# Kernel tuning notes

Measured on AMD Instinct MI355X. Metric: run time of the kernel, lower is better.

## Reference

```python
import jax, jax.numpy as jnp
import numpy as np

N_NODES = 50000
N_EDGES = 800000
F_IN, F_MID, F_OUT = 256, 128, 40


def gcn_conv(x, W, b, src, dst, n_nodes):
    # GCNConv (PyG defaults): add self-loops, symmetric normalization,
    # linear transform, scatter-sum to targets, then bias.
    h = x @ W  # [N, F_out]
    loop = jnp.arange(n_nodes, dtype=src.dtype)
    s = jnp.concatenate([src, loop])  # sources incl. self-loops
    d = jnp.concatenate([dst, loop])  # targets incl. self-loops
    deg = jax.ops.segment_sum(jnp.ones_like(d, dtype=h.dtype), d, num_segments=n_nodes)
    dinv = jnp.where(deg > 0, jax.lax.rsqrt(deg), 0.0)
    norm = dinv[s] * dinv[d]  # [E+N]
    msgs = h[s] * norm[:, None]  # [E+N, F_out]
    out = jax.ops.segment_sum(msgs, d, num_segments=n_nodes)
    return out + b


def setup_inputs() -> dict:
    key = jax.random.key(0)
    ks = jax.random.split(key, 8)
    x = jax.random.normal(ks[0], (N_NODES, F_IN), dtype=jnp.float32)
    edge_index = jax.random.randint(ks[1], (2, N_EDGES), 0, N_NODES, dtype=jnp.int64)

    def glorot(k, fin, fout):
        lim = float(np.sqrt(6.0 / (fin + fout)))
        return jax.random.uniform(k, (fin, fout), jnp.float32, -lim, lim)

    return {
        "x": x,
        "edge_index": edge_index,
        "W_in": glorot(ks[2], F_IN, F_MID),
        "b_in": jnp.zeros((F_MID,), jnp.float32),
        "W_mid": glorot(ks[3], F_MID, F_MID),
        "b_mid": jnp.zeros((F_MID,), jnp.float32),
        "W_out": glorot(ks[4], F_MID, F_OUT),
        "b_out": jnp.zeros((F_OUT,), jnp.float32),
    }


def reference(x, edge_index, W_in, b_in, W_mid, b_mid, W_out, b_out):
    src, dst = edge_index[0], edge_index[1]
    n = x.shape[0]
    # conv_in -> relu (dropout is identity in eval mode)
    h = jax.nn.relu(gcn_conv(x, W_in, b_in, src, dst, n))
    # middle GCN layer -> relu
    h = jax.nn.relu(gcn_conv(h, W_mid, b_mid, src, dst, n))
    # conv_out -> log_softmax over classes
    h = gcn_conv(h, W_out, b_out, src, dst, n)
    return jax.nn.log_softmax(h, axis=-1)
```

## Files before the change

### kernel.cpp

```cpp
#include <hip/hip_runtime.h>
#include <hip/hip_bf16.h>
#include <math.h>


#define F_IN  256
#define F_MID 128
#define F_OUT 40
#define PSH   9
#define BCAP2 10240

typedef __attribute__((ext_vector_type(8))) short bf16x8;
typedef __attribute__((ext_vector_type(4))) float f32x4;

union FragU {
    bf16x8 v;
    __hip_bfloat162 h2[4];
    uint4 u;
    unsigned short s[8];
};

__device__ __forceinline__ unsigned int f2bf(float f) {
    unsigned int u = __float_as_uint(f);
    return (u + 0x7fffu + ((u >> 16) & 1u)) >> 16;
}
__device__ __forceinline__ float bf_lo(unsigned int u) { return __uint_as_float(u << 16); }
__device__ __forceinline__ float bf_hi(unsigned int u) { return __uint_as_float(u & 0xffff0000u); }

__device__ __forceinline__ void add_row(float* acc, uint4 u) {
    acc[0] += bf_lo(u.x); acc[1] += bf_hi(u.x);
    acc[2] += bf_lo(u.y); acc[3] += bf_hi(u.y);
    acc[4] += bf_lo(u.z); acc[5] += bf_hi(u.z);
    acc[6] += bf_lo(u.w); acc[7] += bf_hi(u.w);
}

__global__ __launch_bounds__(256) void k_bucket_prep(const int* __restrict__ src,
                                                     const int* __restrict__ dst,
                                                     unsigned int* __restrict__ bkt,
                                                     int* __restrict__ bcur,
                                                     int E, int nbBkt,
                                                     const float* __restrict__ W1,
                                                     const float* __restrict__ W2,
                                                     const float* __restrict__ W3,
                                                     unsigned short* __restrict__ Wp1,
                                                     unsigned short* __restrict__ Wp2,
                                                     unsigned short* __restrict__ Wp3) {
    if (blockIdx.x >= (unsigned)nbBkt) {
        int t = (blockIdx.x - nbBkt) * 256 + threadIdx.x;
        const float* W; unsigned short* Wp; int M, Mp, kc, nn;
        if (t < 4096)      { W = W1; Wp = Wp1; M = 128; Mp = 128; kc = t >> 7; nn = t & 127; }
        else if (t < 6144) { t -= 4096; W = W2; Wp = Wp2; M = 128; Mp = 128; kc = t >> 7; nn = t & 127; }
        else if (t < 6912) { t -= 6144; W = W3; Wp = Wp3; M = 40;  Mp = 48;  kc = t / 48; nn = t % 48; }
        else return;
        FragU o;
#pragma unroll
        for (int j = 0; j < 8; ++j) {
            int k = kc * 8 + j;
            o.s[j] = (nn < M) ? (unsigned short)f2bf(W[k * M + nn]) : 0;
        }
        *(uint4*)&Wp[((size_t)kc * Mp + nn) * 8] = o.u;
        return;
    }
    __shared__ int hist[128], base[128], cur[128];
    const int t = threadIdx.x;
    if (t < 128) { hist[t] = 0; cur[t] = 0; }
    __syncthreads();
    const int e0 = blockIdx.x * 8192;
    unsigned int mye[32];
#pragma unroll
    for (int j = 0; j < 32; ++j) {
        int e = e0 + j * 256 + t;
        if (e < E) {
            mye[j] = ((unsigned int)dst[e] << 16) | (unsigned int)src[e];
            atomicAdd(&hist[mye[j] >> (16 + PSH)], 1);
        } else mye[j] = 0xffffffffu;
    }
    __syncthreads();
    if (t < 128) base[t] = hist[t] ? atomicAdd(&bcur[t], hist[t]) : 0;
    __syncthreads();
#pragma unroll
    for (int j = 0; j < 32; ++j) {
        if (mye[j] != 0xffffffffu) {
            int p = mye[j] >> (16 + PSH);
            int pos = base[p] + atomicAdd(&cur[p], 1);
            if (pos < BCAP2) bkt[(size_t)p * BCAP2 + pos] = mye[j];
        }
    }
}

__global__ __launch_bounds__(256) void k_sort_pref(const unsigned int* __restrict__ bkt,
                                                   const int* __restrict__ bcur,
                                                   int* __restrict__ rofs,
                                                   float* __restrict__ dinv,
                                                   unsigned short* __restrict__ csr,
                                                   int npart, int n,
                                                   const float* __restrict__ x,
                                                   int nbPref,
                                                   unsigned short* __restrict__ hn1,
                                                   unsigned short* __restrict__ hn2,
                                                   unsigned short* __restrict__ hn3) {
    __shared__ int sh[768];
    if (blockIdx.x >= (unsigned)npart) {
        const int b = blockIdx.x - npart;
        const float4* xp = (const float4*)x;
        const int total4 = n * 64;
        for (int i = b * 256 + threadIdx.x; i < total4; i += nbPref * 256) {
            float4 v = xp[i];
            asm volatile("" :: "v"(v.x), "v"(v.y), "v"(v.z), "v"(v.w));
        }
        return;
    }
    int* hist = sh;
    int* stmp = sh + 512;
    const int p = blockIdx.x;
    const int t = threadIdx.x;
    const int d0 = p << PSH;
    const int nd = min(512, n - d0);

    if (p == 0) {
        uint4 z = make_uint4(0, 0, 0, 0);
        if (t < 16) *(uint4*)(hn1 + (size_t)n * 128 + t * 8) = z;
        else if (t < 32) *(uint4*)(hn2 + (size_t)n * 128 + (t - 16) * 8) = z;
        else if (t < 52) ((unsigned int*)(hn3 + (size_t)n * 40))[t - 32] = 0;
    }

    int bv = (t < p) ? bcur[t] : 0;
    bv = bv > BCAP2 ? BCAP2 : bv;
    stmp[t] = bv;
    hist[t] = 0; hist[t + 256] = 0;
    __syncthreads();
#pragma unroll
    for (int off = 128; off; off >>= 1) {
        if (t < off) stmp[t] += stmp[t + off];
        __syncthreads();
    }
    const int base = stmp[0];
    int np = bcur[p]; np = np > BCAP2 ? BCAP2 : np;
    const unsigned int* b = bkt + (size_t)p * BCAP2;

    for (int i0 = t; i0 < np; i0 += 2048) {
        unsigned int ee[8];
#pragma unroll
        for (int j = 0; j < 8; ++j) {
            int idx = i0 + j * 256;
            ee[j] = (idx < np) ? b[idx] : 0xffffffffu;
        }
#pragma unroll
        for (int j = 0; j < 8; ++j)
            if (ee[j] != 0xffffffffu)
                atomicAdd(&hist[(int)(ee[j] >> 16) - d0], 1);
    }
    __syncthreads();

    const int h0 = hist[2 * t], h1 = hist[2 * t + 1];
    __syncthreads();
    stmp[t] = h0 + h1;
    __syncthreads();
#pragma unroll
    for (int off = 1; off < 256; off <<= 1) {
        int xx = (t >= off) ? stmp[t - off] : 0;
        __syncthreads();
        stmp[t] += xx;
        __syncthreads();
    }
    const int excl = stmp[t] - (h0 + h1);

    hist[2 * t] = excl;
    hist[2 * t + 1] = excl + h0;
    if (2 * t < nd) {
        rofs[d0 + 2 * t] = base + excl;
        dinv[d0 + 2 * t] = rsqrtf((float)(h0 + 1));
    }
    if (2 * t + 1 < nd) {
        rofs[d0 + 2 * t + 1] = base + excl + h0;
        dinv[d0 + 2 * t + 1] = rsqrtf((float)(h1 + 1));
    }
    if (p == npart - 1 && t == 0) rofs[n] = base + np;
    __syncthreads();

    for (int i0 = t; i0 < np; i0 += 2048) {
        unsigned int ee[8];
#pragma unroll
        for (int j = 0; j < 8; ++j) {
            int idx = i0 + j * 256;
            ee[j] = (idx < np) ? b[idx] : 0xffffffffu;
        }
#pragma unroll
        for (int j = 0; j < 8; ++j) {
            if (ee[j] != 0xffffffffu) {
                int ld = (int)(ee[j] >> 16) - d0;
                int pos = atomicAdd(&hist[ld], 1);
                csr[base + pos] = (unsigned short)(ee[j] & 0xffffu);
            }
        }
    }
}

__global__ __launch_bounds__(256) void k_gemm1s(const float* __restrict__ x,
                                                const unsigned short* __restrict__ Wp1,
                                                const float* __restrict__ dinv,
                                                unsigned short* __restrict__ hn, int n) {
    const int t = threadIdx.x;
    const int w = t >> 6, lane = t & 63, sub = lane & 15, q = lane >> 4;
    const int row0 = blockIdx.x * 64 + w * 16;
    const int row = row0 + sub;
    const bool rv = row < n;
    const float* ap = x + (size_t)row * 256;

    float4 xv[16];
    if (rv) {
#pragma unroll
        for (int j = 0; j < 16; ++j)
            xv[j] = *(const float4*)(ap + (j >> 1) * 32 + q * 8 + (j & 1) * 4);
    } else {
#pragma unroll
        for (int j = 0; j < 16; ++j) xv[j] = make_float4(0.f, 0.f, 0.f, 0.f);
    }

    f32x4 acc[8];
#pragma unroll
    for (int cg = 0; cg < 8; ++cg) acc[cg] = (f32x4)0.f;

#pragma unroll
    for (int kk = 0; kk < 8; ++kk) {
        FragU af;
        float4 f0 = xv[2 * kk];
        float4 f1 = xv[2 * kk + 1];
        af.h2[0] = __float22bfloat162_rn(make_float2(f0.x, f0.y));
        af.h2[1] = __float22bfloat162_rn(make_float2(f0.z, f0.w));
        af.h2[2] = __float22bfloat162_rn(make_float2(f1.x, f1.y));
        af.h2[3] = __float22bfloat162_rn(make_float2(f1.z, f1.w));
        const unsigned short* wrow = Wp1 + (size_t)((kk * 4 + q) * 128 + sub) * 8;
#pragma unroll
        for (int cg = 0; cg < 8; ++cg) {
            bf16x8 b = *(const bf16x8*)(wrow + cg * 16 * 8);
            acc[cg] = __builtin_amdgcn_mfma_f32_16x16x32_bf16(b, af.v, acc[cg], 0, 0, 0);
        }
    }
    if (rv) {
        float dv = dinv[row];
#pragma unroll
        for (int cg = 0; cg < 8; ++cg) {
            uint2 pk;
            pk.x = f2bf(dv * acc[cg][0]) | (f2bf(dv * acc[cg][1]) << 16);
            pk.y = f2bf(dv * acc[cg][2]) | (f2bf(dv * acc[cg][3]) << 16);
            *(uint2*)(hn + (size_t)row * 128 + cg * 16 + q * 4) = pk;
        }
    }
}

template <int MOUT, int MP>
__global__ __launch_bounds__(256) void k_agg_gemm(const unsigned short* __restrict__ hnS,
                                                  const int* __restrict__ rofs,
                                                  const unsigned short* __restrict__ csr,
                                                  const float* __restrict__ dinv,
                                                  const float* __restrict__ bias,
                                                  const unsigned short* __restrict__ Wp,
                                                  unsigned short* __restrict__ hout,
                                                  int n) {
    __shared__ unsigned short arows[16][136];
    const int t = threadIdx.x;
    const int w = t >> 6, lane = t & 63, sub = lane & 15, q = lane >> 4;
    const int v0 = blockIdx.x * 16;
    const int r = w * 4 + q;
    const int node = v0 + r;
    const bool nv = node < n;

    float acc[8];
#pragma unroll
    for (int k = 0; k < 8; ++k) acc[k] = 0.f;

    int e0 = 0, deg = 0;
    if (nv) { e0 = rofs[node]; deg = rofs[node + 1] - e0; }
    const int total = nv ? deg + 1 : 0;
    int ea = (sub < deg) ? (int)csr[e0 + sub] : n;
    int eb = (16 + sub < deg) ? (int)csr[e0 + 16 + sub] : n;
    const int lim = (total < 33) ? total : 33;

    for (int ix0 = 0; ix0 < lim; ix0 += 8) {
        int sA[8];
#pragma unroll
        for (int jj = 0; jj < 8; ++jj) {
            int ix = ix0 + jj;
            int em = (ix - 1) & 15;
            int srcA = __shfl(ea, (lane & 48) + em);
            int srcB = __shfl(eb, (lane & 48) + em);
            int s = (ix - 1 < 16) ? srcA : srcB;
            s = (ix == 0) ? node : s;
            sA[jj] = (ix < lim) ? s : n;
        }
        uint4 u[8];
#pragma unroll
        for (int jj = 0; jj < 8; ++jj)
            u[jj] = *(const uint4*)(hnS + (size_t)sA[jj] * 128 + sub * 8);
#pragma unroll
        for (int jj = 0; jj < 8; ++jj) add_row(acc, u[jj]);
    }
    for (int ix = 33; ix < total; ++ix) {
        int s = (int)csr[e0 + ix - 1];
        uint4 u = *(const uint4*)(hnS + (size_t)s * 128 + sub * 8);
        add_row(acc, u);
    }

    uint4 pk = make_uint4(0, 0, 0, 0);
    if (nv) {
        float dv = dinv[node];
        float4 b0 = *(const float4*)(bias + sub * 8);
        float4 b1 = *(const float4*)(bias + sub * 8 + 4);
        float o0 = fmaxf(dv * acc[0] + b0.x, 0.f);
        float o1 = fmaxf(dv * acc[1] + b0.y, 0.f);
        float o2 = fmaxf(dv * acc[2] + b0.z, 0.f);
        float o3 = fmaxf(dv * acc[3] + b0.w, 0.f);
        float o4 = fmaxf(dv * acc[4] + b1.x, 0.f);
        float o5 = fmaxf(dv * acc[5] + b1.y, 0.f);
        float o6 = fmaxf(dv * acc[6] + b1.z, 0.f);
        float o7 = fmaxf(dv * acc[7] + b1.w, 0.f);
        pk.x = f2bf(o0) | (f2bf(o1) << 16);
        pk.y = f2bf(o2) | (f2bf(o3) << 16);
        pk.z = f2bf(o4) | (f2bf(o5) << 16);
        pk.w = f2bf(o6) | (f2bf(o7) << 16);
    }
    *(uint4*)&arows[r][sub * 8] = pk;
    __syncthreads();

    const int NCG = MP / 16;
    const int NCGW = (MP == 128) ? 2 : 1;
    f32x4 gacc[2];
#pragma unroll
    for (int i = 0; i < 2; ++i) gacc[i] = (f32x4)0.f;

#pragma unroll
    for (int kstep = 0; kstep < 4; ++kstep) {
        FragU af;
        af.u = *(const uint4*)&arows[sub][kstep * 32 + q * 8];
#pragma unroll
        for (int i = 0; i < NCGW; ++i) {
            int cg = w * NCGW + i;
            if (cg < NCG) {
                bf16x8 b = *(const bf16x8*)(Wp + (size_t)((kstep * 4 + q) * MP + cg * 16 + sub) * 8);
                gacc[i] = __builtin_amdgcn_mfma_f32_16x16x32_bf16(b, af.v, gacc[i], 0, 0, 0);
            }
        }
    }
    const int orow = v0 + sub;
    if (orow < n) {
        float dvr = dinv[orow];
#pragma unroll
        for (int i = 0; i < NCGW; ++i) {
            int cg = w * NCGW + i;
            int feat = cg * 16 + q * 4;
            if (cg < NCG && feat < MOUT) {
                uint2 p2;
                p2.x = f2bf(dvr * gacc[i][0]) | (f2bf(dvr * gacc[i][1]) << 16);
                p2.y = f2bf(dvr * gacc[i][2]) | (f2bf(dvr * gacc[i][3]) << 16);
                *(uint2*)(hout + (size_t)orow * MOUT + feat) = p2;
            }
        }
    }
}

__global__ __launch_bounds__(256) void agg40_lsm_bf16(const unsigned short* __restrict__ hnS,
                                                      const int* __restrict__ rofs,
                                                      const unsigned short* __restrict__ csr,
                                                      const float* __restrict__ dinv,
                                                      const float* __restrict__ bias,
                                                      float* __restrict__ out, int n) {
    int wid = (blockIdx.x * 256 + threadIdx.x) >> 6;
    if (wid >= n) return;
    const int v = wid;
    const int lane = threadIdx.x & 63;
    const int h = lane >> 5;
    const int sl = lane & 31;
    const bool act = sl < 20;
    float a0 = 0.f, a1 = 0.f;
    const int e0 = rofs[v];
    const int total = rofs[v + 1] - e0 + 1;

    for (int i0 = 0; i0 < total; i0 += 16) {
        int sA[8];
#pragma unroll
        for (int j = 0; j < 8; ++j) {
            int ix = i0 + h + 2 * j;
            int s = (ix < total) ? ((ix == 0) ? v : (int)csr[e0 + ix - 1]) : n;
            sA[j] = s;
        }
        if (act) {
#pragma unroll
            for (int j = 0; j < 8; ++j) {
                unsigned int u = *(const unsigned int*)(hnS + (size_t)sA[j] * 40 + sl * 2);
                a0 += bf_lo(u);
                a1 += bf_hi(u);
            }
        }
    }
    a0 += __shfl_xor(a0, 32);
    a1 += __shfl_xor(a1, 32);
    float dv = dinv[v];
    float v0 = act ? (dv * a0 + bias[sl * 2])     : -3.402823466e38f;
    float v1 = act ? (dv * a1 + bias[sl * 2 + 1]) : -3.402823466e38f;
    float m = fmaxf(v0, v1);
#pragma unroll
    for (int off = 16; off; off >>= 1) m = fmaxf(m, __shfl_xor(m, off));
    float p = act ? (__expf(v0 - m) + __expf(v1 - m)) : 0.f;
#pragma unroll
    for (int off = 16; off; off >>= 1) p += __shfl_xor(p, off);
    if (h == 0 && act) {
        float ls = __logf(p);
        *(float2*)(out + (size_t)v * 40 + sl * 2) = make_float2(v0 - m - ls, v1 - m - ls);
    }
}


extern "C" void kernel_launch(void* const* d_in, const int* in_sizes, int n_in,
                              void* d_out, int out_size, void* d_ws, size_t ws_size,
                              hipStream_t stream) {
    const float* x     = (const float*)d_in[0];
    const int*   ei    = (const int*)d_in[1];
    const float* W_in  = (const float*)d_in[2];
    const float* b_in  = (const float*)d_in[3];
    const float* W_mid = (const float*)d_in[4];
    const float* b_mid = (const float*)d_in[5];
    const float* W_out = (const float*)d_in[6];
    const float* b_out = (const float*)d_in[7];
    float* out = (float*)d_out;

    const int N = in_sizes[0] / F_IN;
    const int E = in_sizes[1] / 2;
    const int* srcp = ei;
    const int* dstp = ei + E;
    const int npart = (N + (1 << PSH) - 1) >> PSH;

    char* w = (char*)d_ws;
    unsigned short* hn1 = (unsigned short*)w; w += (size_t)(N + 1) * 128 * 2;
    unsigned short* hn2 = (unsigned short*)w; w += (size_t)(N + 1) * 128 * 2;
    unsigned short* hn3 = (unsigned short*)w; w += (size_t)(N + 1) * 40 * 2 + 16;
    float* dinv = (float*)w; w += (size_t)N * 4;
    int* bcur   = (int*)w;   w += 512;
    int* rofs   = (int*)w;   w += (size_t)(N + 1) * 4 + 12;
    unsigned int* bkt = (unsigned int*)w; w += (size_t)npart * BCAP2 * 4;
    unsigned short* csr = (unsigned short*)w; w += (size_t)E * 2 + 128;
    unsigned short* Wp1 = (unsigned short*)((((size_t)w) + 15) & ~(size_t)15); w = (char*)Wp1 + 32 * 128 * 8 * 2;
    unsigned short* Wp2 = (unsigned short*)w; w += 16 * 128 * 8 * 2;
    unsigned short* Wp3 = (unsigned short*)w; w += 16 * 48 * 8 * 2;

    const int nbW = (N * 64 + 255) / 256;
    const int nbG = (N + 63) / 64;
    const int nbF = (N + 15) / 16;
    const int nbBkt = (E + 8191) / 8192;
    const int nbPref = 256;

    hipMemsetAsync(bcur, 0, 512, stream);
    k_bucket_prep<<<nbBkt + 27, 256, 0, stream>>>(srcp, dstp, bkt, bcur, E, nbBkt,
                                                  W_in, W_mid, W_out, Wp1, Wp2, Wp3);
    k_sort_pref<<<npart + nbPref, 256, 0, stream>>>(bkt, bcur, rofs, dinv, csr,
                                                    npart, N, x, nbPref, hn1, hn2, hn3);
    k_gemm1s<<<nbG, 256, 0, stream>>>(x, Wp1, dinv, hn1, N);
    k_agg_gemm<128, 128><<<nbF, 256, 0, stream>>>(hn1, rofs, csr, dinv, b_in, Wp2, hn2, N);
    k_agg_gemm<40, 48><<<nbF, 256, 0, stream>>>(hn2, rofs, csr, dinv, b_mid, Wp3, hn3, N);
    agg40_lsm_bf16<<<nbW, 256, 0, stream>>>(hn3, rofs, csr, dinv, b_out, out, N);
}
```

Before: 244.6 us.

## Fuse CSR sort with first GEMM using a device-wide completion flag

Merges the sort kernel and the first-layer GEMM into one launch. Sort blocks signal completion through an atomic counter. GEMM blocks compute their MFMA products first, then spin until every sort block has finished before scaling rows by dinv and storing. This replaces the old x-prefetch blocks with real overlap of the GEMM and the sort, and removes one launch. It relies on the sort blocks being scheduled ahead of or alongside the waiting blocks; spinning blocks hold compute slots while they wait.

```diff
diff --git a/kernel.cpp b/kernel.cpp
--- a/kernel.cpp
+++ b/kernel.cpp
@@ -87,121 +87,111 @@
     }
 }
 
-__global__ __launch_bounds__(256) void k_sort_pref(const unsigned int* __restrict__ bkt,
-                                                   const int* __restrict__ bcur,
-                                                   int* __restrict__ rofs,
-                                                   float* __restrict__ dinv,
-                                                   unsigned short* __restrict__ csr,
-                                                   int npart, int n,
-                                                   const float* __restrict__ x,
-                                                   int nbPref,
-                                                   unsigned short* __restrict__ hn1,
-                                                   unsigned short* __restrict__ hn2,
-                                                   unsigned short* __restrict__ hn3) {
+__global__ __launch_bounds__(256) void k_sort_gemm1(const unsigned int* __restrict__ bkt,
+                                                    const int* __restrict__ bcur,
+                                                    int* __restrict__ rofs,
+                                                    float* __restrict__ dinv,
+                                                    unsigned short* __restrict__ csr,
+                                                    int* __restrict__ sortdone,
+                                                    int npart, int n,
+                                                    const float* __restrict__ x,
+                                                    const unsigned short* __restrict__ Wp1,
+                                                    unsigned short* __restrict__ hn1,
+                                                    unsigned short* __restrict__ hn2,
+                                                    unsigned short* __restrict__ hn3) {
     __shared__ int sh[768];
-    if (blockIdx.x >= (unsigned)npart) {
-        const int b = blockIdx.x - npart;
-        const float4* xp = (const float4*)x;
-        const int total4 = n * 64;
-        for (int i = b * 256 + threadIdx.x; i < total4; i += nbPref * 256) {
-            float4 v = xp[i];
-            asm volatile("" :: "v"(v.x), "v"(v.y), "v"(v.z), "v"(v.w));
-        }
+    if (blockIdx.x < (unsigned)npart) {
+        int* hist = sh;
+        int* stmp = sh + 512;
+        const int p = blockIdx.x;
+        const int t = threadIdx.x;
+        const int d0 = p << PSH;
+        const int nd = min(512, n - d0);
+
+        if (p == 0) {
+            uint4 z = make_uint4(0, 0, 0, 0);
+            if (t < 16) *(uint4*)(hn1 + (size_t)n * 128 + t * 8) = z;
+            else if (t < 32) *(uint4*)(hn2 + (size_t)n * 128 + (t - 16) * 8) = z;
+            else if (t < 52) ((unsigned int*)(hn3 + (size_t)n * 40))[t - 32] = 0;
+        }
+
+        int bv = (t < p) ? bcur[t] : 0;
+        bv = bv > BCAP2 ? BCAP2 : bv;
+        stmp[t] = bv;
+        hist[t] = 0; hist[t + 256] = 0;
+        __syncthreads();
+#pragma unroll
+        for (int off = 128; off; off >>= 1) {
+            if (t < off) stmp[t] += stmp[t + off];
+            __syncthreads();
+        }
+        const int base = stmp[0];
+        int np = bcur[p]; np = np > BCAP2 ? BCAP2 : np;
+        const unsigned int* b = bkt + (size_t)p * BCAP2;
+
+        for (int i0 = t; i0 < np; i0 += 2048) {
+            unsigned int ee[8];
+#pragma unroll
+            for (int j = 0; j < 8; ++j) {
+                int idx = i0 + j * 256;
+                ee[j] = (idx < np) ? b[idx] : 0xffffffffu;
+            }
+#pragma unroll
+            for (int j = 0; j < 8; ++j)
+                if (ee[j] != 0xffffffffu)
+                    atomicAdd(&hist[(int)(ee[j] >> 16) - d0], 1);
+        }
+        __syncthreads();
+
+        const int h0 = hist[2 * t], h1 = hist[2 * t + 1];
+        __syncthreads();
+        stmp[t] = h0 + h1;
+        __syncthreads();
+#pragma unroll
+        for (int off = 1; off < 256; off <<= 1) {
+            int xx = (t >= off) ? stmp[t - off] : 0;
+            __syncthreads();
+            stmp[t] += xx;
+            __syncthreads();
+        }
+        const int excl = stmp[t] - (h0 + h1);
+
+        hist[2 * t] = excl;
+        hist[2 * t + 1] = excl + h0;
+        if (2 * t < nd) {
+            rofs[d0 + 2 * t] = base + excl;
+            dinv[d0 + 2 * t] = rsqrtf((float)(h0 + 1));
+        }
+        if (2 * t + 1 < nd) {
+            rofs[d0 + 2 * t + 1] = base + excl + h0;
+            dinv[d0 + 2 * t + 1] = rsqrtf((float)(h1 + 1));
+        }
+        if (p == npart - 1 && t == 0) rofs[n] = base + np;
+        __syncthreads();
+
+        for (int i0 = t; i0 < np; i0 += 2048) {
+            unsigned int ee[8];
+#pragma unroll
+            for (int j = 0; j < 8; ++j) {
+                int idx = i0 + j * 256;
+                ee[j] = (idx < np) ? b[idx] : 0xffffffffu;
+            }
+#pragma unroll
+            for (int j = 0; j < 8; ++j) {
+                if (ee[j] != 0xffffffffu) {
+                    int ld = (int)(ee[j] >> 16) - d0;
+                    int pos = atomicAdd(&hist[ld], 1);
+                    csr[base + pos] = (unsigned short)(ee[j] & 0xffffu);
+                }
+            }
+        }
+        __syncthreads();
+        if (t == 0) { __threadfence(); atomicAdd(sortdone, 1); }
         return;
     }
-    int* hist = sh;
-    int* stmp = sh + 512;
-    const int p = blockIdx.x;
-    const int t = threadIdx.x;
-    const int d0 = p << PSH;
-    const int nd = min(512, n - d0);
-
-    if (p == 0) {
-        uint4 z = make_uint4(0, 0, 0, 0);
-        if (t < 16) *(uint4*)(hn1 + (size_t)n * 128 + t * 8) = z;
-        else if (t < 32) *(uint4*)(hn2 + (size_t)n * 128 + (t - 16) * 8) = z;
-        else if (t < 52) ((unsigned int*)(hn3 + (size_t)n * 40))[t - 32] = 0;
-    }
-
-    int bv = (t < p) ? bcur[t] : 0;
-    bv = bv > BCAP2 ? BCAP2 : bv;
-    stmp[t] = bv;
-    hist[t] = 0; hist[t + 256] = 0;
-    __syncthreads();
-#pragma unroll
-    for (int off = 128; off; off >>= 1) {
-        if (t < off) stmp[t] += stmp[t + off];
-        __syncthreads();
-    }
-    const int base = stmp[0];
-    int np = bcur[p]; np = np > BCAP2 ? BCAP2 : np;
-    const unsigned int* b = bkt + (size_t)p * BCAP2;
-
-    for (int i0 = t; i0 < np; i0 += 2048) {
-        unsigned int ee[8];
-#pragma unroll
-        for (int j = 0; j < 8; ++j) {
-            int idx = i0 + j * 256;
-            ee[j] = (idx < np) ? b[idx] : 0xffffffffu;
-        }
-#pragma unroll
-        for (int j = 0; j < 8; ++j)
-            if (ee[j] != 0xffffffffu)
-                atomicAdd(&hist[(int)(ee[j] >> 16) - d0], 1);
-    }
-    __syncthreads();
-
-    const int h0 = hist[2 * t], h1 = hist[2 * t + 1];
-    __syncthreads();
-    stmp[t] = h0 + h1;
-    __syncthreads();
-#pragma unroll
-    for (int off = 1; off < 256; off <<= 1) {
-        int xx = (t >= off) ? stmp[t - off] : 0;
-        __syncthreads();
-        stmp[t] += xx;
-        __syncthreads();
-    }
-    const int excl = stmp[t] - (h0 + h1);
-
-    hist[2 * t] = excl;
-    hist[2 * t + 1] = excl + h0;
-    if (2 * t < nd) {
-        rofs[d0 + 2 * t] = base + excl;
-        dinv[d0 + 2 * t] = rsqrtf((float)(h0 + 1));
-    }
-    if (2 * t + 1 < nd) {
-        rofs[d0 + 2 * t + 1] = base + excl + h0;
-        dinv[d0 + 2 * t + 1] = rsqrtf((float)(h1 + 1));
-    }
-    if (p == npart - 1 && t == 0) rofs[n] = base + np;
-    __syncthreads();
-
-    for (int i0 = t; i0 < np; i0 += 2048) {
-        unsigned int ee[8];
-#pragma unroll
-        for (int j = 0; j < 8; ++j) {
-            int idx = i0 + j * 256;
-            ee[j] = (idx < np) ? b[idx] : 0xffffffffu;
-        }
-#pragma unroll
-        for (int j = 0; j < 8; ++j) {
-            if (ee[j] != 0xffffffffu) {
-                int ld = (int)(ee[j] >> 16) - d0;
-                int pos = atomicAdd(&hist[ld], 1);
-                csr[base + pos] = (unsigned short)(ee[j] & 0xffffu);
-            }
-        }
-    }
-}
-
-__global__ __launch_bounds__(256) void k_gemm1s(const float* __restrict__ x,
-                                                const unsigned short* __restrict__ Wp1,
-                                                const float* __restrict__ dinv,
-                                                unsigned short* __restrict__ hn, int n) {
     const int t = threadIdx.x;
     const int w = t >> 6, lane = t & 63, sub = lane & 15, q = lane >> 4;
-    const int row0 = blockIdx.x * 64 + w * 16;
+    const int row0 = (blockIdx.x - npart) * 64 + w * 16;
     const int row = row0 + sub;
     const bool rv = row < n;
     const float* ap = x + (size_t)row * 256;
@@ -236,6 +226,11 @@
             acc[cg] = __builtin_amdgcn_mfma_f32_16x16x32_bf16(b, af.v, acc[cg], 0, 0, 0);
         }
     }
+    if (t == 0) {
+        while (__hip_atomic_load(sortdone, __ATOMIC_ACQUIRE, __HIP_MEMORY_SCOPE_AGENT) < npart)
+            __builtin_amdgcn_s_sleep(8);
+    }
+    __syncthreads();
     if (rv) {
         float dv = dinv[row];
 #pragma unroll
@@ -243,7 +238,7 @@
             uint2 pk;
             pk.x = f2bf(dv * acc[cg][0]) | (f2bf(dv * acc[cg][1]) << 16);
             pk.y = f2bf(dv * acc[cg][2]) | (f2bf(dv * acc[cg][3]) << 16);
-            *(uint2*)(hn + (size_t)row * 128 + cg * 16 + q * 4) = pk;
+            *(uint2*)(hn1 + (size_t)row * 128 + cg * 16 + q * 4) = pk;
         }
     }
 }
@@ -434,26 +429,26 @@
     unsigned short* hn2 = (unsigned short*)w; w += (size_t)(N + 1) * 128 * 2;
     unsigned short* hn3 = (unsigned short*)w; w += (size_t)(N + 1) * 40 * 2 + 16;
     float* dinv = (float*)w; w += (size_t)N * 4;
-    int* bcur   = (int*)w;   w += 512;
+    int* bcur   = (int*)w;   w += 1024;
     int* rofs   = (int*)w;   w += (size_t)(N + 1) * 4 + 12;
     unsigned int* bkt = (unsigned int*)w; w += (size_t)npart * BCAP2 * 4;
     unsigned short* csr = (unsigned short*)w; w += (size_t)E * 2 + 128;
     unsigned short* Wp1 = (unsigned short*)((((size_t)w) + 15) & ~(size_t)15); w = (char*)Wp1 + 32 * 128 * 8 * 2;
     unsigned short* Wp2 = (unsigned short*)w; w += 16 * 128 * 8 * 2;
     unsigned short* Wp3 = (unsigned short*)w; w += 16 * 48 * 8 * 2;
+    int* sortdone = bcur + 128;
 
     const int nbW = (N * 64 + 255) / 256;
     const int nbG = (N + 63) / 64;
     const int nbF = (N + 15) / 16;
     const int nbBkt = (E + 8191) / 8192;
-    const int nbPref = 256;
-
-    hipMemsetAsync(bcur, 0, 512, stream);
+
+    hipMemsetAsync(bcur, 0, 1024, stream);
     k_bucket_prep<<<nbBkt + 27, 256, 0, stream>>>(srcp, dstp, bkt, bcur, E, nbBkt,
                                                   W_in, W_mid, W_out, Wp1, Wp2, Wp3);
-    k_sort_pref<<<npart + nbPref, 256, 0, stream>>>(bkt, bcur, rofs, dinv, csr,
-                                                    npart, N, x, nbPref, hn1, hn2, hn3);
-    k_gemm1s<<<nbG, 256, 0, stream>>>(x, Wp1, dinv, hn1, N);
+    k_sort_gemm1<<<npart + nbG, 256, 0, stream>>>(bkt, bcur, rofs, dinv, csr,
+                                                  sortdone, npart, N,
+                                                  x, Wp1, hn1, hn2, hn3);
     k_agg_gemm<128, 128><<<nbF, 256, 0, stream>>>(hn1, rofs, csr, dinv, b_in, Wp2, hn2, N);
     k_agg_gemm<40, 48><<<nbF, 256, 0, stream>>>(hn2, rofs, csr, dinv, b_mid, Wp3, hn3, N);
     agg40_lsm_bf16<<<nbW, 256, 0, stream>>>(hn3, rofs, csr, dinv, b_out, out, N);
```

New measurement: 320.8 us. 1.31x slower.
